# Performance work log

Measured on AMD Instinct MI355X. Metric: run time of the kernel, lower is better.

The kernel has to match this reference:

```python
import jax, jax.numpy as jnp
import numpy as np

B, N_SITES, N_SYMM, FEATS, LAYERS = 1024, 256, 256, 32, 4


def setup_inputs() -> dict:
    key = jax.random.key(0)
    k1, k2, k3, k4, k5 = jax.random.split(key, 5)
    x_in = jax.random.normal(k1, (B, N_SITES), jnp.float32)
    # Cyclic translation group C_{N_SITES}: perm_g(i) = (i + g) mod N
    i = jnp.arange(N_SITES)
    g = jnp.arange(N_SYMM)
    perms = (i[None, :] + g[:, None]) % N_SITES              # [n_symm, n_sites] int
    # Cayley-table style algebra index: alg[gi, go] = (go - gi) mod n_symm
    group_algebra = ((g[None, :] - g[:, None]) % N_SYMM).reshape(-1)  # [n_symm^2]
    w_symm = jax.random.normal(k2, (N_SITES, FEATS), jnp.float32) / np.sqrt(N_SITES).astype(np.float32)
    b_symm = jax.random.normal(k3, (FEATS,), jnp.float32) * 0.01
    w_eq = jax.random.normal(k4, (LAYERS - 1, N_SYMM, FEATS, FEATS), jnp.float32) / np.sqrt(N_SYMM * FEATS).astype(np.float32)
    b_eq = jax.random.normal(k5, (LAYERS - 1, FEATS), jnp.float32) * 0.01
    return dict(x_in=x_in, perms=perms, group_algebra=group_algebra,
                w_symm=w_symm, b_symm=b_symm, w_eq=w_eq, b_eq=b_eq)


def reference(x_in, perms, group_algebra, w_symm, b_symm, w_eq, b_eq):
    n_symm, n_sites = perms.shape
    feats = w_symm.shape[1]
    # --- DenseSymm: K[g, i, f] = w_symm[perms[g, i], f]  (permutation gather)
    K = jnp.take(w_symm, perms, axis=0)                      # [n_symm, n_sites, feats]
    # y[b, f, g] = sum_i x[b, i] * K[g, i, f] + b_symm[f]
    x = jnp.einsum('bi,gif->bfg', x_in, K) + b_symm[None, :, None]  # [B, feats, n_symm]
    alg = group_algebra.reshape(n_symm, n_symm)              # [gi, go]
    n_layers = w_eq.shape[0]
    for l in range(n_layers):
        # full kernel: Kl[gi, go, fi, fo] = w_eq[l, alg[gi, go], fi, fo]
        Kl = jnp.take(w_eq[l], alg, axis=0)                  # [n_symm, n_symm, feats, feats]
        x = jnp.einsum('bfg,ghfo->boh', x, Kl) + b_eq[l][None, :, None]
        x = jax.nn.swish(x)
    # mean over the flattened (features * n_symm) hidden axis
    return jnp.mean(x, axis=(-2, -1))                        # [B]
```

## Files before the change

kernel.cpp:

```cpp
#include <hip/hip_runtime.h>


#define NG 256
#define KB 129
#define NLAYER 3
#define SLAB 4130

__device__ __forceinline__ int brv6(int x) { return (int)(__brev((unsigned)x) >> 26); }

__device__ __forceinline__ int swz(int a) {
  int h = a >> 4;
  return a ^ ((h ^ (h << 1)) & 15);
}

__device__ __forceinline__ void wave_fft256_lds(float2* __restrict__ s,
                                                const float2* __restrict__ tw,
                                                int lane) {
  asm volatile("s_waitcnt lgkmcnt(0)" ::: "memory");
  #pragma unroll
  for (int t = 0; t < 4; ++t) {
    int i = t * 64 + lane;
    int j = (int)(__brev((unsigned)i) >> 24);
    if (j > i) {
      float2 a = s[swz(i)]; float2 b = s[swz(j)];
      s[swz(i)] = b; s[swz(j)] = a;
    }
  }
  asm volatile("s_waitcnt lgkmcnt(0)" ::: "memory");
  #pragma unroll
  for (int st = 0; st < 8; ++st) {
    const int half = 1 << st;
    const int tshift = 7 - st;
    #pragma unroll
    for (int t = 0; t < 2; ++t) {
      int bf = t * 64 + lane;
      int off = bf & (half - 1);
      int blk = bf >> st;
      int i = (blk << (st + 1)) + off;
      int j = i + half;
      float2 wv = tw[swz(off << tshift)];
      float2 u = s[swz(i)];
      float2 v = s[swz(j)];
      float vr = v.x * wv.x - v.y * wv.y;
      float vi = v.x * wv.y + v.y * wv.x;
      s[swz(i)] = make_float2(u.x + vr, u.y + vi);
      s[swz(j)] = make_float2(u.x - vr, u.y - vi);
    }
    asm volatile("s_waitcnt lgkmcnt(0)" ::: "memory");
  }
}

__global__ __launch_bounds__(256) void gcnn_wfft(
    const float* __restrict__ w_symm, const float* __restrict__ w_eq,
    float2* __restrict__ Ws_hat, float2* __restrict__ Weq_hat) {
  __shared__ float2 fbw[4][256];
  __shared__ float2 twl[256];
  const int tid = threadIdx.x;
  const int w = tid >> 6;
  const int lane = tid & 63;
  {
    float a = (float)tid * 0.0245436926f;
    twl[swz(tid)] = make_float2(cosf(a), -sinf(a));
  }
  __syncthreads();
  const int task = blockIdx.x * 4 + w;
  if (task < 32) {
    const int f = task;
    for (int g = lane; g < 256; g += 64)
      fbw[w][swz(g)] = make_float2(w_symm[g * 32 + f], 0.f);
    wave_fft256_lds(&fbw[w][0], twl, lane);
    for (int k = lane; k < KB; k += 64) {
      int sk = (k < 64) ? brv6(k) : ((k < 128) ? 64 + brv6(k - 64) : 128);
      Ws_hat[f * KB + sk] = fbw[w][swz(k)];
    }
  } else {
    const int idx = task - 32;
    const int l = idx >> 10;
    const int fi = (idx >> 5) & 31;
    const int fo = idx & 31;
    for (int g = lane; g < 256; g += 64)
      fbw[w][swz(g)] = make_float2(w_eq[((size_t)(l * 256 + g) * 32 + fi) * 32 + fo] * (1.f / 256.f), 0.f);
    wave_fft256_lds(&fbw[w][0], twl, lane);
    for (int k = lane; k < KB; k += 64) {
      int sk = (k < 64) ? brv6(k) : ((k < 128) ? 64 + brv6(k - 64) : 128);
      Weq_hat[((size_t)((l * 32 + fi) * KB + sk)) * 32 + fo] = fbw[w][swz(k)];
    }
  }
}

__device__ __forceinline__ float2 cadd(float2 a, float2 b) { return make_float2(a.x + b.x, a.y + b.y); }
__device__ __forceinline__ float2 csub(float2 a, float2 b) { return make_float2(a.x - b.x, a.y - b.y); }
__device__ __forceinline__ float2 cmul(float2 a, float2 b) {
  return make_float2(a.x * b.x - a.y * b.y, a.x * b.y + a.y * b.x);
}
__device__ __forceinline__ float2 cmulc(float2 a, float2 b) {
  return make_float2(a.x * b.x + a.y * b.y, a.y * b.x - a.x * b.y);
}
__device__ __forceinline__ float2 shxor(float2 v, int m) {
  return make_float2(__shfl_xor(v.x, m), __shfl_xor(v.y, m));
}

__device__ __forceinline__ void fwd256(float2 z[4], const float2 tw[5],
                                       float2 u1, float2 u2, float2 u3, int lane) {
  #pragma unroll
  for (int s = 0; s < 6; ++s) {
    const int half = 32 >> s;
    const bool bot = (lane & half) != 0;
    #pragma unroll
    for (int r = 0; r < 4; ++r) {
      float2 o = shxor(z[r], half);
      float2 sum = cadd(z[r], o);
      float2 dif = csub(o, z[r]);
      float2 bo = (s < 5) ? cmul(dif, tw[s]) : dif;
      z[r] = bot ? bo : sum;
    }
  }
  z[1] = cmul(z[1], u1);
  z[2] = cmul(z[2], u2);
  z[3] = cmul(z[3], u3);
  float2 t0 = cadd(z[0], z[2]), t1 = cadd(z[1], z[3]);
  float2 t2 = csub(z[0], z[2]), t3 = csub(z[1], z[3]);
  z[0] = cadd(t0, t1);
  z[2] = csub(t0, t1);
  z[1] = make_float2(t2.x + t3.y, t2.y - t3.x);
  z[3] = make_float2(t2.x - t3.y, t2.y + t3.x);
}

__device__ __forceinline__ void inv256(float2 z[4], const float2 tw[5],
                                       float2 u1, float2 u2, float2 u3, int lane) {
  float2 t0 = cadd(z[0], z[2]), t1 = cadd(z[1], z[3]);
  float2 t2 = csub(z[0], z[2]), t3 = csub(z[1], z[3]);
  z[0] = cadd(t0, t1);
  z[2] = csub(t0, t1);
  z[1] = make_float2(t2.x - t3.y, t2.y + t3.x);
  z[3] = make_float2(t2.x + t3.y, t2.y - t3.x);
  z[1] = cmulc(z[1], u1);
  z[2] = cmulc(z[2], u2);
  z[3] = cmulc(z[3], u3);
  #pragma unroll
  for (int s = 5; s >= 0; --s) {
    const int half = 32 >> s;
    const bool bot = (lane & half) != 0;
    #pragma unroll
    for (int r = 0; r < 4; ++r) {
      float2 m = (s < 5 && bot) ? cmulc(z[r], tw[s]) : z[r];
      float2 o = shxor(m, half);
      z[r] = bot ? csub(o, m) : cadd(o, m);
    }
  }
}

__device__ __forceinline__ float2 zdir(float2 A, float2 B) {
  return make_float2(A.x - B.y, A.y + B.x);
}
__device__ __forceinline__ float2 zconj(float2 A, float2 B) {
  return make_float2(A.x + B.y, B.x - A.y);
}
__device__ __forceinline__ float swishf(float y) { return y / (1.f + __expf(-y)); }

__global__ __launch_bounds__(512, 1) void gcnn_main(
    const float* __restrict__ x_in, const float* __restrict__ b_symm,
    const float* __restrict__ b_eq, const float2* __restrict__ Ws_hat,
    const float2* __restrict__ Weq_hat, float* __restrict__ out) {
  __shared__ float2 Hs[4 * SLAB];
  __shared__ float2 fx[4][132];
  __shared__ float red[8][4];

  const int tid = threadIdx.x;
  const int w = tid >> 6;
  const int lane = tid & 63;
  const int brev = brv6(lane);

  float2 tw[5];
  #pragma unroll
  for (int s = 0; s < 5; ++s) {
    const int half = 32 >> s;
    float ang = -0.09817477042468103871f * (float)((lane & (half - 1)) << s);
    __sincosf(ang, &tw[s].y, &tw[s].x);
  }
  float2 u1;
  {
    float ang = -0.02454369260617025968f * (float)brev;
    __sincosf(ang, &u1.y, &u1.x);
  }
  const float2 u2 = cmul(u1, u1);
  const float2 u3 = cmul(u2, u1);
  const int rb = brv6((64 - brev) & 63);
  const int s2 = (brev == 0) ? 128 : 64 + rb;
  const int s3 = (brev == 0) ? 64 : rb;

  if (w < 4) {
    float4 xv = reinterpret_cast<const float4*>(x_in + (size_t)(blockIdx.x * 4 + w) * NG)[lane];
    float2 z[4] = {{xv.x, 0.f}, {xv.y, 0.f}, {xv.z, 0.f}, {xv.w, 0.f}};
    fwd256(z, tw, u1, u2, u3, lane);
    fx[w][lane] = z[0];
    fx[w][64 + lane] = z[1];
    if (lane == 0) fx[w][128] = z[2];
  }
  __syncthreads();

  for (int t = w; t < 128; t += 8) {
    const int r = t >> 5;
    const int f = t & 31;
    const float bs = 256.f * b_symm[f];
    const float2* wsf = Ws_hat + f * KB;
    float2* hrow = Hs + r * SLAB + f * KB;
    for (int s = lane; s < KB; s += 64) {
      float2 xk = fx[r][s];
      float2 wv = wsf[s];
      float2 rr = make_float2(xk.x * wv.x + xk.y * wv.y,
                              xk.x * wv.y - xk.y * wv.x);
      if (s == 0) rr.x += bs;
      hrow[s] = rr;
    }
  }
  __syncthreads();

  #pragma unroll 1
  for (int l = 0; l < NLAYER; ++l) {
    const bool last = (l == NLAYER - 1);

    {
      const int r = tid & 3;
      const int s = tid >> 2;
      float2 acc[32];
      #pragma unroll
      for (int fo = 0; fo < 32; ++fo) acc[fo] = make_float2(0.f, 0.f);
      const float2* hcol = Hs + r * SLAB + s;
      #pragma unroll 2
      for (int fi = 0; fi < 32; ++fi) {
        float2 h = hcol[fi * KB];
        const float4* wp = reinterpret_cast<const float4*>(
            Weq_hat + ((size_t)((l * 32 + fi) * KB + s)) * 32);
        #pragma unroll
        for (int q = 0; q < 16; ++q) {
          float4 v = wp[q];
          acc[2 * q].x     += h.x * v.x - h.y * v.y;
          acc[2 * q].y     += h.x * v.y + h.y * v.x;
          acc[2 * q + 1].x += h.x * v.z - h.y * v.w;
          acc[2 * q + 1].y += h.x * v.w + h.y * v.z;
        }
      }
      float2* hw = Hs + r * SLAB + s;
      if (s == 0) {
        #pragma unroll
        for (int fo = 0; fo < 32; ++fo) acc[fo].x += b_eq[l * 32 + fo];
      }
      #pragma unroll
      for (int fo = 0; fo < 32; ++fo) hw[fo * KB] = acc[fo];
      if (w == 0) {
        #pragma unroll
        for (int jj = 0; jj < 2; ++jj) {
          const int rr = (lane >> 5) + 2 * jj;
          const int fo = lane & 31;
          const float2* hc = Hs + rr * SLAB + 128;
          float2 a = make_float2(0.f, 0.f);
          #pragma unroll 4
          for (int fi = 0; fi < 32; ++fi) {
            float2 h = hc[fi * KB];
            float2 v = Weq_hat[((size_t)((l * 32 + fi) * KB + 128)) * 32 + fo];
            a.x += h.x * v.x - h.y * v.y;
            a.y += h.x * v.y + h.y * v.x;
          }
          (Hs + rr * SLAB + 128)[fo * KB] = a;
        }
      }
    }
    __syncthreads();

    #pragma unroll
    for (int rr = 0; rr < 4; ++rr) {
      float lsr = 0.f;
      for (int p = w; p < 16; p += 8) {
        float2* rA = Hs + rr * SLAB + (2 * p) * KB;
        float2* rB = rA + KB;
        float2 z[4];
        {
          float2 A0 = rA[lane],      B0 = rB[lane];
          float2 A1 = rA[64 + lane], B1 = rB[64 + lane];
          float2 A2 = rA[s2],        B2 = rB[s2];
          float2 A3 = rA[s3],        B3 = rB[s3];
          z[0] = zdir(A0, B0);
          z[1] = zdir(A1, B1);
          z[2] = (brev == 0) ? zdir(A2, B2) : zconj(A2, B2);
          z[3] = zconj(A3, B3);
        }
        inv256(z, tw, u1, u2, u3, lane);
        if (!last) {
          #pragma unroll
          for (int r4 = 0; r4 < 4; ++r4) {
            z[r4].x = swishf(z[r4].x);
            z[r4].y = swishf(z[r4].y);
          }
          fwd256(z, tw, u1, u2, u3, lane);
          float2 M0 = make_float2(__shfl(z[3].x, rb), __shfl(z[3].y, rb));
          float2 M1 = make_float2(__shfl(z[2].x, rb), __shfl(z[2].y, rb));
          float2 M2 = make_float2(__shfl(z[1].x, rb), __shfl(z[1].y, rb));
          if (brev == 0) { M0 = z[0]; M1 = z[3]; M2 = z[2]; }
          float2 A0 = make_float2(0.5f * (z[0].x + M0.x), 0.5f * (z[0].y - M0.y));
          float2 B0 = make_float2(0.5f * (z[0].y + M0.y), 0.5f * (M0.x - z[0].x));
          float2 A1 = make_float2(0.5f * (z[1].x + M1.x), 0.5f * (z[1].y - M1.y));
          float2 B1 = make_float2(0.5f * (z[1].y + M1.y), 0.5f * (M1.x - z[1].x));
          rA[lane] = A0;       rB[lane] = B0;
          rA[64 + lane] = A1;  rB[64 + lane] = B1;
          if (lane == 0) {
            float2 A2 = make_float2(0.5f * (z[2].x + M2.x), 0.5f * (z[2].y - M2.y));
            float2 B2 = make_float2(0.5f * (z[2].y + M2.y), 0.5f * (M2.x - z[2].x));
            rA[128] = A2;
            rB[128] = B2;
          }
        } else {
          #pragma unroll
          for (int r4 = 0; r4 < 4; ++r4)
            lsr += swishf(z[r4].x) + swishf(z[r4].y);
        }
      }
      if (last) {
        lsr += __shfl_xor(lsr, 32);
        lsr += __shfl_xor(lsr, 16);
        lsr += __shfl_xor(lsr, 8);
        lsr += __shfl_xor(lsr, 4);
        lsr += __shfl_xor(lsr, 2);
        lsr += __shfl_xor(lsr, 1);
        if (lane == 0) red[w][rr] = lsr;
      }
    }
    __syncthreads();
  }

  if (tid < 4) {
    float s = 0.f;
    #pragma unroll
    for (int ww = 0; ww < 8; ++ww) s += red[ww][tid];
    out[blockIdx.x * 4 + tid] = s * (1.f / 8192.f);
  }
}

extern "C" void kernel_launch(void* const* d_in, const int* in_sizes, int n_in,
                              void* d_out, int out_size, void* d_ws, size_t ws_size,
                              hipStream_t stream) {
  const float* x_in   = (const float*)d_in[0];
  const float* w_symm = (const float*)d_in[3];
  const float* b_symm = (const float*)d_in[4];
  const float* w_eq   = (const float*)d_in[5];
  const float* b_eq   = (const float*)d_in[6];
  float* out = (float*)d_out;

  float2* Ws_hat  = (float2*)d_ws;
  float2* Weq_hat = Ws_hat + 32 * KB;

  hipLaunchKernelGGL(gcnn_wfft, dim3(776), dim3(256), 0, stream,
                     w_symm, w_eq, Ws_hat, Weq_hat);
  hipLaunchKernelGGL(gcnn_main, dim3(256), dim3(512), 0, stream,
                     x_in, b_symm, b_eq, Ws_hat, Weq_hat, out);
}
```

Before: 187.6 us.

## Halve samples per block and split output features across thread pairs

Each block of gcnn_main now handles 2 batch samples instead of 4, and the grid doubles to 512 blocks so more of the GPU is occupied. In the spectral mixing step each thread computes 16 output features instead of 32, with two threads sharing a frequency bin and sample, which cuts accumulator register pressure. The Nyquist bin (index 128) is moved out of the main weight layout into its own buffer and a small LDS array. The main transformed weights use a stride of 128, so the loads stay aligned. The cost is that each weight load is reused across fewer samples, so global and L2 traffic for the weights per sample roughly doubles.

```diff
diff --git a/kernel.cpp b/kernel.cpp
--- a/kernel.cpp
+++ b/kernel.cpp
@@ -3,8 +3,9 @@
 
 #define NG 256
 #define KB 129
+#define FSTR 129
+#define SLAB (32 * FSTR + 2)
 #define NLAYER 3
-#define SLAB 4130
 
 __device__ __forceinline__ int brv6(int x) { return (int)(__brev((unsigned)x) >> 26); }
 
@@ -52,7 +53,8 @@
 
 __global__ __launch_bounds__(256) void gcnn_wfft(
     const float* __restrict__ w_symm, const float* __restrict__ w_eq,
-    float2* __restrict__ Ws_hat, float2* __restrict__ Weq_hat) {
+    float2* __restrict__ Ws_hat, float2* __restrict__ WeqM,
+    float2* __restrict__ Weq128) {
   __shared__ float2 fbw[4][256];
   __shared__ float2 twl[256];
   const int tid = threadIdx.x;
@@ -69,7 +71,7 @@
     for (int g = lane; g < 256; g += 64)
       fbw[w][swz(g)] = make_float2(w_symm[g * 32 + f], 0.f);
     wave_fft256_lds(&fbw[w][0], twl, lane);
-    for (int k = lane; k < KB; k += 64) {
+    for (int k = lane; k < 129; k += 64) {
       int sk = (k < 64) ? brv6(k) : ((k < 128) ? 64 + brv6(k - 64) : 128);
       Ws_hat[f * KB + sk] = fbw[w][swz(k)];
     }
@@ -81,9 +83,12 @@
     for (int g = lane; g < 256; g += 64)
       fbw[w][swz(g)] = make_float2(w_eq[((size_t)(l * 256 + g) * 32 + fi) * 32 + fo] * (1.f / 256.f), 0.f);
     wave_fft256_lds(&fbw[w][0], twl, lane);
-    for (int k = lane; k < KB; k += 64) {
+    for (int k = lane; k < 129; k += 64) {
       int sk = (k < 64) ? brv6(k) : ((k < 128) ? 64 + brv6(k - 64) : 128);
-      Weq_hat[((size_t)((l * 32 + fi) * KB + sk)) * 32 + fo] = fbw[w][swz(k)];
+      if (sk < 128)
+        WeqM[((size_t)((l * 32 + fi) * 128 + sk)) * 32 + fo] = fbw[w][swz(k)];
+      else
+        Weq128[(l * 32 + fi) * 32 + fo] = fbw[w][swz(k)];
     }
   }
 }
@@ -161,10 +166,12 @@
 __global__ __launch_bounds__(512, 1) void gcnn_main(
     const float* __restrict__ x_in, const float* __restrict__ b_symm,
     const float* __restrict__ b_eq, const float2* __restrict__ Ws_hat,
-    const float2* __restrict__ Weq_hat, float* __restrict__ out) {
-  __shared__ float2 Hs[4 * SLAB];
-  __shared__ float2 fx[4][132];
-  __shared__ float red[8][4];
+    const float2* __restrict__ WeqM, const float2* __restrict__ Weq128,
+    float* __restrict__ out) {
+  __shared__ float2 Hs[2 * SLAB];
+  __shared__ float2 b128s[2 * 32];
+  __shared__ float2 fx[2][132];
+  __shared__ float red[8][2];
 
   const int tid = threadIdx.x;
   const int w = tid >> 6;
@@ -186,11 +193,11 @@
   const float2 u2 = cmul(u1, u1);
   const float2 u3 = cmul(u2, u1);
   const int rb = brv6((64 - brev) & 63);
-  const int s2 = (brev == 0) ? 128 : 64 + rb;
+  const int s2 = 64 + rb;
   const int s3 = (brev == 0) ? 64 : rb;
 
-  if (w < 4) {
-    float4 xv = reinterpret_cast<const float4*>(x_in + (size_t)(blockIdx.x * 4 + w) * NG)[lane];
+  if (w < 2) {
+    float4 xv = reinterpret_cast<const float4*>(x_in + (size_t)(blockIdx.x * 2 + w) * NG)[lane];
     float2 z[4] = {{xv.x, 0.f}, {xv.y, 0.f}, {xv.z, 0.f}, {xv.w, 0.f}};
     fwd256(z, tw, u1, u2, u3, lane);
     fx[w][lane] = z[0];
@@ -199,19 +206,20 @@
   }
   __syncthreads();
 
-  for (int t = w; t < 128; t += 8) {
+  for (int t = w; t < 64; t += 8) {
     const int r = t >> 5;
     const int f = t & 31;
     const float bs = 256.f * b_symm[f];
     const float2* wsf = Ws_hat + f * KB;
-    float2* hrow = Hs + r * SLAB + f * KB;
-    for (int s = lane; s < KB; s += 64) {
+    float2* hrow = Hs + r * SLAB + f * FSTR;
+    for (int s = lane; s < 129; s += 64) {
       float2 xk = fx[r][s];
       float2 wv = wsf[s];
       float2 rr = make_float2(xk.x * wv.x + xk.y * wv.y,
                               xk.x * wv.y - xk.y * wv.x);
       if (s == 0) rr.x += bs;
-      hrow[s] = rr;
+      if (s < 128) hrow[s] = rr;
+      else b128s[r * 32 + f] = rr;
     }
   }
   __syncthreads();
@@ -221,19 +229,20 @@
     const bool last = (l == NLAYER - 1);
 
     {
-      const int r = tid & 3;
       const int s = tid >> 2;
-      float2 acc[32];
+      const int r = (tid >> 1) & 1;
+      const int hf = tid & 1;
+      float2 acc[16];
       #pragma unroll
-      for (int fo = 0; fo < 32; ++fo) acc[fo] = make_float2(0.f, 0.f);
+      for (int j = 0; j < 16; ++j) acc[j] = make_float2(0.f, 0.f);
       const float2* hcol = Hs + r * SLAB + s;
       #pragma unroll 2
       for (int fi = 0; fi < 32; ++fi) {
-        float2 h = hcol[fi * KB];
+        float2 h = hcol[fi * FSTR];
         const float4* wp = reinterpret_cast<const float4*>(
-            Weq_hat + ((size_t)((l * 32 + fi) * KB + s)) * 32);
+            WeqM + ((size_t)((l * 32 + fi) * 128 + s)) * 32 + hf * 16);
         #pragma unroll
-        for (int q = 0; q < 16; ++q) {
+        for (int q = 0; q < 8; ++q) {
           float4 v = wp[q];
           acc[2 * q].x     += h.x * v.x - h.y * v.y;
           acc[2 * q].y     += h.x * v.y + h.y * v.x;
@@ -241,45 +250,48 @@
           acc[2 * q + 1].y += h.x * v.w + h.y * v.z;
         }
       }
-      float2* hw = Hs + r * SLAB + s;
       if (s == 0) {
         #pragma unroll
-        for (int fo = 0; fo < 32; ++fo) acc[fo].x += b_eq[l * 32 + fo];
-      }
+        for (int j = 0; j < 16; ++j) acc[j].x += b_eq[l * 32 + hf * 16 + j];
+      }
+      float2* hw = Hs + r * SLAB + s;
       #pragma unroll
-      for (int fo = 0; fo < 32; ++fo) hw[fo * KB] = acc[fo];
+      for (int j = 0; j < 16; ++j) hw[(hf * 16 + j) * FSTR] = acc[j];
       if (w == 0) {
-        #pragma unroll
-        for (int jj = 0; jj < 2; ++jj) {
-          const int rr = (lane >> 5) + 2 * jj;
-          const int fo = lane & 31;
-          const float2* hc = Hs + rr * SLAB + 128;
-          float2 a = make_float2(0.f, 0.f);
-          #pragma unroll 4
-          for (int fi = 0; fi < 32; ++fi) {
-            float2 h = hc[fi * KB];
-            float2 v = Weq_hat[((size_t)((l * 32 + fi) * KB + 128)) * 32 + fo];
-            a.x += h.x * v.x - h.y * v.y;
-            a.y += h.x * v.y + h.y * v.x;
-          }
-          (Hs + rr * SLAB + 128)[fo * KB] = a;
+        const int rr = lane >> 5;
+        const int fo = lane & 31;
+        float2 a = make_float2(0.f, 0.f);
+        #pragma unroll 4
+        for (int fi = 0; fi < 32; ++fi) {
+          float2 h = b128s[rr * 32 + fi];
+          float2 v = Weq128[(l * 32 + fi) * 32 + fo];
+          a.x += h.x * v.x - h.y * v.y;
+          a.y += h.x * v.y + h.y * v.x;
         }
+        b128s[rr * 32 + fo] = a;
       }
     }
     __syncthreads();
 
     #pragma unroll
-    for (int rr = 0; rr < 4; ++rr) {
+    for (int rr = 0; rr < 2; ++rr) {
       float lsr = 0.f;
       for (int p = w; p < 16; p += 8) {
-        float2* rA = Hs + rr * SLAB + (2 * p) * KB;
-        float2* rB = rA + KB;
+        float2* rA = Hs + rr * SLAB + (2 * p) * FSTR;
+        float2* rB = rA + FSTR;
         float2 z[4];
         {
           float2 A0 = rA[lane],      B0 = rB[lane];
           float2 A1 = rA[64 + lane], B1 = rB[64 + lane];
-          float2 A2 = rA[s2],        B2 = rB[s2];
-          float2 A3 = rA[s3],        B3 = rB[s3];
+          float2 A2, B2;
+          if (brev == 0) {
+            A2 = b128s[rr * 32 + 2 * p];
+            B2 = b128s[rr * 32 + 2 * p + 1];
+          } else {
+            A2 = rA[s2];
+            B2 = rB[s2];
+          }
+          float2 A3 = rA[s3], B3 = rB[s3];
           z[0] = zdir(A0, B0);
           z[1] = zdir(A1, B1);
           z[2] = (brev == 0) ? zdir(A2, B2) : zconj(A2, B2);
@@ -306,8 +318,8 @@
           if (lane == 0) {
             float2 A2 = make_float2(0.5f * (z[2].x + M2.x), 0.5f * (z[2].y - M2.y));
             float2 B2 = make_float2(0.5f * (z[2].y + M2.y), 0.5f * (M2.x - z[2].x));
-            rA[128] = A2;
-            rB[128] = B2;
+            b128s[rr * 32 + 2 * p] = A2;
+            b128s[rr * 32 + 2 * p + 1] = B2;
           }
         } else {
           #pragma unroll
@@ -328,11 +340,11 @@
     __syncthreads();
   }
 
-  if (tid < 4) {
+  if (tid < 2) {
     float s = 0.f;
     #pragma unroll
     for (int ww = 0; ww < 8; ++ww) s += red[ww][tid];
-    out[blockIdx.x * 4 + tid] = s * (1.f / 8192.f);
+    out[blockIdx.x * 2 + tid] = s * (1.f / 8192.f);
   }
 }
 
@@ -346,11 +358,12 @@
   const float* b_eq   = (const float*)d_in[6];
   float* out = (float*)d_out;
 
-  float2* Ws_hat  = (float2*)d_ws;
-  float2* Weq_hat = Ws_hat + 32 * KB;
+  float2* Ws_hat = (float2*)d_ws;
+  float2* WeqM   = Ws_hat + 32 * KB;
+  float2* Weq128 = WeqM + (size_t)3 * 32 * 128 * 32;
 
   hipLaunchKernelGGL(gcnn_wfft, dim3(776), dim3(256), 0, stream,
-                     w_symm, w_eq, Ws_hat, Weq_hat);
-  hipLaunchKernelGGL(gcnn_main, dim3(256), dim3(512), 0, stream,
-                     x_in, b_symm, b_eq, Ws_hat, Weq_hat, out);
-}
+                     w_symm, w_eq, Ws_hat, WeqM, Weq128);
+  hipLaunchKernelGGL(gcnn_main, dim3(512), dim3(512), 0, stream,
+                     x_in, b_symm, b_eq, Ws_hat, WeqM, Weq128, out);
+}
```

New measurement: 269.5 us. 43.6% more time.
